# Kernel tuning notes

Hardware: AMD Instinct MI355X
Metric: run time of the kernel (lower is better)

## Reference

```python
import jax, jax.numpy as jnp
import numpy as np

B, N, C = 1, 131072, 128
BS, H = 32, 4          # block_size, num_heads
HD = C // H            # head_dim = 32
NB = N // BS           # num_blocks = 4096
NEG = -1e30            # stand-in for -inf (identical softmax result, safe grads)


def setup_inputs() -> dict:
    key = jax.random.key(0)
    ks = jax.random.split(key, 8)
    x = jax.random.normal(ks[0], (B, N, C), jnp.float32)
    edge_feats = jax.random.normal(ks[1], (NB, BS, BS + 1, 4), jnp.float32)
    # 0/1 connectivity mask; guarantee self (diagonal) and global-token column are attendable
    attn_mask = jax.random.randint(ks[2], (NB, BS, BS + 1), 0, 2).astype(jnp.int32)
    attn_mask = attn_mask.at[:, :, BS].set(1)
    d = jnp.arange(BS)
    attn_mask = attn_mask.at[:, d, d].set(1)
    # parameters (torch nn.Linear layout: weight [out, in])
    Wqkv = jax.random.normal(ks[3], (3 * C, C), jnp.float32) * (C ** -0.5)
    bqkv = jnp.zeros((3 * C,), jnp.float32)
    Wproj = jax.random.normal(ks[4], (C, C), jnp.float32) * (C ** -0.5)
    bproj = jnp.zeros((C,), jnp.float32)
    Wgate = jax.random.normal(ks[5], (H, 4), jnp.float32) * 0.01  # init std=0.01
    bgate = jnp.zeros((H,), jnp.float32)
    return dict(x=x, edge_feats=edge_feats, Wqkv=Wqkv, bqkv=bqkv,
                Wproj=Wproj, bproj=bproj, Wgate=Wgate, bgate=bgate,
                attn_mask=attn_mask)


def reference(x, edge_feats, Wqkv, bqkv, Wproj, bproj, Wgate, bgate, attn_mask):
    scale = HD ** -0.5
    x_blk = x.reshape(B, NB, BS, C)
    # global token per block = block mean
    block_node = x_blk.mean(axis=2, keepdims=True)          # [B,NB,1,C]
    kv = jnp.concatenate([x_blk, block_node], axis=2)       # [B,NB,BS+1,C]
    # qkv projections (slice the fused weight like the torch code slices outputs)
    q = (x_blk @ Wqkv[:C].T + bqkv[:C]).reshape(B, NB, BS, H, HD)
    k = (kv @ Wqkv[C:2 * C].T + bqkv[C:2 * C]).reshape(B, NB, BS + 1, H, HD)
    v = (kv @ Wqkv[2 * C:].T + bqkv[2 * C:]).reshape(B, NB, BS + 1, H, HD)
    scores = jnp.einsum('bnqhd,bnkhd->bnqkh', q, k) * scale  # [B,NB,BS,BS+1,H]
    # physics bias: overwrite global-token column and diagonal with (0,0,0,1)
    self_row = jnp.array([0.0, 0.0, 0.0, 1.0], jnp.float32)
    bp = jnp.broadcast_to(edge_feats[None], (B, NB, BS, BS + 1, 4))
    bp = bp.at[:, :, :, BS, :].set(self_row)
    d = jnp.arange(BS)
    bp = bp.at[:, :, d, d, :].set(self_row)
    scores = scores + bp[..., 3:4]                           # additive physics bias
    m = attn_mask[None, :, :, :, None] != 0                  # [1,NB,BS,BS+1,1]
    scores = jnp.where(m, scores, NEG)
    attn_probs = jax.nn.softmax(scores, axis=3)
    # additive edge gate (masked to 0 where disconnected)
    lew = jnp.where(m, bp @ Wgate.T + bgate, 0.0)            # [B,NB,BS,BS+1,H]
    combined = attn_probs + lew
    x_out = jnp.einsum('bnqkh,bnkhd->bnqhd', combined, v).reshape(B, N, C)
    return x_out @ Wproj.T + bproj
```

## Files before the change

### kernel.cpp

```cpp
#include <hip/hip_runtime.h>
#include <hip/hip_bf16.h>

#define NBLK 4096
#define BS 32
#define CH 128

typedef float f32x4 __attribute__((ext_vector_type(4)));
typedef int   i32x4 __attribute__((ext_vector_type(4)));
typedef short bf16x8 __attribute__((ext_vector_type(8)));
typedef unsigned short u16x4 __attribute__((ext_vector_type(4)));

__device__ __forceinline__ short f2b(float x) {
    return __builtin_bit_cast(short, __float2bfloat16(x));
}
__device__ __forceinline__ float b2f(unsigned short h) {
    union { unsigned u; float f; } c; c.u = ((unsigned)h) << 16; return c.f;
}
__device__ __forceinline__ u16x4 pack4(f32x4 a) {
    u16x4 o;
    o[0] = (unsigned short)f2b(a[0]); o[1] = (unsigned short)f2b(a[1]);
    o[2] = (unsigned short)f2b(a[2]); o[3] = (unsigned short)f2b(a[3]);
    return o;
}
__device__ __forceinline__ bf16x8 pack8(f32x4 a, f32x4 b) {
    bf16x8 o;
    o[0] = f2b(a[0]); o[1] = f2b(a[1]); o[2] = f2b(a[2]); o[3] = f2b(a[3]);
    o[4] = f2b(b[0]); o[5] = f2b(b[1]); o[6] = f2b(b[2]); o[7] = f2b(b[3]);
    return o;
}
__device__ __forceinline__ int swz(int row, int col) {
    return (row << 5) + ((((col >> 3) ^ ((row >> 1) & 3)) << 3) | (col & 7));
}

__global__ void convert_weights(const float* __restrict__ wqkv,
                                const float* __restrict__ wproj,
                                short* __restrict__ wsout) {
    int i = blockIdx.x * 256 + threadIdx.x;
    if (i < 3 * CH * CH) {
        wsout[i] = f2b(wqkv[i]);
    } else {
        int j = i - 3 * CH * CH;
        if (j < CH * CH) wsout[3 * CH * CH + j] = f2b(wproj[j]);
    }
}

__launch_bounds__(256, 3)
__global__ void fused_block_attn(
    const float* __restrict__ x,
    const float* __restrict__ edge_feats,
    const float* __restrict__ bqkv,
    const float* __restrict__ bproj,
    const float* __restrict__ wgate,
    const float* __restrict__ bgate,
    const int*   __restrict__ attn_mask,
    const short* __restrict__ wqkv_b,
    const short* __restrict__ wproj_b,
    float* __restrict__ out)
{
    const int b    = blockIdx.x;
    const int tid  = threadIdx.x;
    const int lane = tid & 63;
    const int w    = tid >> 6;
    const int lm   = lane & 15;
    const int g    = lane >> 4;
    const int ak   = g * 8;
    const int rb   = g * 4;

    __shared__ short Rv[4096];
    __shared__ short Rq[4096];
    __shared__ short Rk[4096];
    __shared__ short efS[4096];
    short* vt = Rv + w * 1024;
    short* qc = Rq + w * 1024;
    short* kc = Rk + w * 1024;

    const int pr = tid >> 3;
    const int pu = tid & 7;
    const float* efp = edge_feats + ((size_t)(b * BS + pr) * 33 + pu * 4) * 4;
    f32x4 efv[4];
    efv[0] = ((const f32x4*)efp)[0];
    efv[1] = ((const f32x4*)efp)[1];
    efv[2] = ((const f32x4*)efp)[2];
    efv[3] = ((const f32x4*)efp)[3];
    const i32x4 mkv = *(const i32x4*)(attn_mask + (size_t)(b * BS + pr) * 33 + pu * 4);

    const float* xb = x + (size_t)b * (BS * CH);
    bf16x8 kvf[2][4];
    #pragma unroll
    for (int kk = 0; kk < 4; ++kk) {
        const float* p0 = xb + lm * CH + kk * 32 + ak;
        const float* p1 = p0 + 16 * CH;
        kvf[0][kk] = pack8(*(const f32x4*)p0, *(const f32x4*)(p0 + 4));
        kvf[1][kk] = pack8(*(const f32x4*)p1, *(const f32x4*)(p1 + 4));
    }

    bf16x8 wfa[4][4];
    #pragma unroll
    for (int t = 0; t < 4; ++t) {
        const int o0 = ((t >> 1) ? CH : 0) + w * 32 + (t & 1) * 16;
        const short* wp = wqkv_b + (o0 + lm) * CH + ak;
        #pragma unroll
        for (int kk = 0; kk < 4; ++kk) wfa[t][kk] = *(const bf16x8*)(wp + kk * 32);
    }
    #pragma unroll
    for (int t = 0; t < 4; ++t) {
        const int o0 = ((t >> 1) ? CH : 0) + w * 32 + (t & 1) * 16;
        f32x4 acc0 = *(const f32x4*)(bqkv + o0 + rb);
        f32x4 acc1 = acc0;
        #pragma unroll
        for (int kk = 0; kk < 4; ++kk) {
            acc0 = __builtin_amdgcn_mfma_f32_16x16x32_bf16(wfa[t][kk], kvf[0][kk], acc0, 0, 0, 0);
            acc1 = __builtin_amdgcn_mfma_f32_16x16x32_bf16(wfa[t][kk], kvf[1][kk], acc1, 0, 0, 0);
        }
        short* dst = (t >> 1) ? kc : qc;
        const int c0 = (t & 1) * 16 + rb;
        *(u16x4*)&dst[swz(lm, c0)]      = pack4(acc0);
        *(u16x4*)&dst[swz(16 + lm, c0)] = pack4(acc1);
    }
    #pragma unroll
    for (int t = 0; t < 2; ++t) {
        const int o0 = 2 * CH + w * 32 + t * 16;
        const short* wp = wqkv_b + (o0 + lm) * CH + ak;
        bf16x8 wf[4];
        #pragma unroll
        for (int kk = 0; kk < 4; ++kk) wf[kk] = *(const bf16x8*)(wp + kk * 32);
        float bv = bqkv[o0 + lm];
        f32x4 acc0 = {bv, bv, bv, bv};
        f32x4 acc1 = acc0;
        #pragma unroll
        for (int kk = 0; kk < 4; ++kk) {
            acc0 = __builtin_amdgcn_mfma_f32_16x16x32_bf16(kvf[0][kk], wf[kk], acc0, 0, 0, 0);
            acc1 = __builtin_amdgcn_mfma_f32_16x16x32_bf16(kvf[1][kk], wf[kk], acc1, 0, 0, 0);
        }
        const int row = t * 16 + lm;
        *(u16x4*)&vt[swz(row, rb)]      = pack4(acc0);
        *(u16x4*)&vt[swz(row, 16 + rb)] = pack4(acc1);
    }

    {
        #pragma unroll
        for (int jj = 0; jj < 2; ++jj) {
            bf16x8 st;
            #pragma unroll
            for (int h2 = 0; h2 < 2; ++h2) {
                const int s = pu * 4 + jj * 2 + h2;
                f32x4 e = efv[jj * 2 + h2];
                if (s == pr) { e[0] = 0.f; e[1] = 0.f; e[2] = 0.f; e[3] = 1.f; }
                const float e3 = mkv[jj * 2 + h2] ? e[3] : -INFINITY;
                st[h2 * 4 + 0] = f2b(e[0]);
                st[h2 * 4 + 1] = f2b(e[1]);
                st[h2 * 4 + 2] = f2b(e[2]);
                st[h2 * 4 + 3] = f2b(e3);
            }
            const int chunk = pu * 2 + jj;
            *(bf16x8*)&efS[pr * 128 + ((chunk ^ (pr & 15)) << 3)] = st;
        }
    }
    __syncthreads();

    {
        bf16x8 af0 = *(const bf16x8*)&kc[swz(lm, ak)];
        bf16x8 af1 = *(const bf16x8*)&kc[swz(16 + lm, ak)];
        bf16x8 bq0 = *(const bf16x8*)&qc[swz(lm, ak)];
        bf16x8 bq1 = *(const bf16x8*)&qc[swz(16 + lm, ak)];
        f32x4 z = {0.f, 0.f, 0.f, 0.f};
        f32x4 s00 = __builtin_amdgcn_mfma_f32_16x16x32_bf16(af0, bq0, z, 0, 0, 0);
        f32x4 s10 = __builtin_amdgcn_mfma_f32_16x16x32_bf16(af1, bq0, z, 0, 0, 0);
        f32x4 s01 = __builtin_amdgcn_mfma_f32_16x16x32_bf16(af0, bq1, z, 0, 0, 0);
        f32x4 s11 = __builtin_amdgcn_mfma_f32_16x16x32_bf16(af1, bq1, z, 0, 0, 0);
        const float SC = 0.17677669529663689f;
        *(u16x4*)&kc[swz(lm, rb)]           = pack4(s00 * SC);
        *(u16x4*)&kc[swz(lm, 16 + rb)]      = pack4(s10 * SC);
        *(u16x4*)&kc[swz(16 + lm, rb)]      = pack4(s01 * SC);
        *(u16x4*)&kc[swz(16 + lm, 16 + rb)] = pack4(s11 * SC);
    }

    {
        const int r    = lane >> 1;
        const int half = lane & 1;
        bf16x8 t0 = *(const bf16x8*)&kc[swz(r, half * 16)];
        bf16x8 t1 = *(const bf16x8*)&kc[swz(r, half * 16 + 8)];

        float dv[16];
        #pragma unroll
        for (int j = 0; j < 8; ++j) {
            dv[j]     = b2f((unsigned short)t0[j]);
            dv[8 + j] = b2f((unsigned short)t1[j]);
        }
        float sd = 0.f;
        #pragma unroll
        for (int j = 0; j < 16; ++j) sd += dv[j];
        sd += __shfl_xor(sd, 1);
        const float d32 = sd * 0.03125f;

        f32x4 wg = *(const f32x4*)(wgate + w * 4);
        float bg = bgate[w];

        float e[16], lw[16];
        float se = 0.f;
        #pragma unroll
        for (int pk = 0; pk < 8; ++pk) {
            const int chunk = half * 8 + pk;
            bf16x8 c = *(const bf16x8*)&efS[r * 128 + ((chunk ^ (r & 15)) << 3)];
            #pragma unroll
            for (int h2 = 0; h2 < 2; ++h2) {
                const int idx = pk * 2 + h2;
                const float f0 = b2f((unsigned short)c[h2 * 4 + 0]);
                const float f1 = b2f((unsigned short)c[h2 * 4 + 1]);
                const float f2c = b2f((unsigned short)c[h2 * 4 + 2]);
                const float f3 = b2f((unsigned short)c[h2 * 4 + 3]);
                const bool m = f3 > -1.0e30f;
                lw[idx] = m ? (f0 * wg[0] + f1 * wg[1] + f2c * wg[2] + f3 * wg[3] + bg) : 0.f;
                e[idx]  = __expf(dv[idx] + f3);
                se += e[idx];
            }
        }
        const float e32 = __expf(d32 + 1.0f);
        const float tot = se + __shfl_xor(se, 1) + e32;
        const float rinv = 1.0f / tot;
        const float add32 = (e32 * rinv + wg[3] + bg) * 0.03125f;

        #pragma unroll
        for (int pk = 0; pk < 4; ++pk) {
            f32x4 v;
            #pragma unroll
            for (int j = 0; j < 4; ++j) {
                int idx = pk * 4 + j;
                v[j] = e[idx] * rinv + lw[idx] + add32;
            }
            *(u16x4*)&kc[swz(r, half * 16 + pk * 4)] = pack4(v);
        }
    }

    {
        bf16x8 av0 = *(const bf16x8*)&vt[swz(lm, ak)];
        bf16x8 av1 = *(const bf16x8*)&vt[swz(16 + lm, ak)];
        bf16x8 bc0 = *(const bf16x8*)&kc[swz(lm, ak)];
        bf16x8 bc1 = *(const bf16x8*)&kc[swz(16 + lm, ak)];
        f32x4 z = {0.f, 0.f, 0.f, 0.f};
        f32x4 x00 = __builtin_amdgcn_mfma_f32_16x16x32_bf16(av0, bc0, z, 0, 0, 0);
        f32x4 x10 = __builtin_amdgcn_mfma_f32_16x16x32_bf16(av1, bc0, z, 0, 0, 0);
        f32x4 x01 = __builtin_amdgcn_mfma_f32_16x16x32_bf16(av0, bc1, z, 0, 0, 0);
        f32x4 x11 = __builtin_amdgcn_mfma_f32_16x16x32_bf16(av1, bc1, z, 0, 0, 0);
        *(u16x4*)&qc[swz(lm, rb)]           = pack4(x00);
        *(u16x4*)&qc[swz(lm, 16 + rb)]      = pack4(x10);
        *(u16x4*)&qc[swz(16 + lm, rb)]      = pack4(x01);
        *(u16x4*)&qc[swz(16 + lm, 16 + rb)] = pack4(x11);
    }

    bf16x8 pw[2][4];
    float pb[2];
    #pragma unroll
    for (int t = 0; t < 2; ++t) {
        int col = w * 32 + t * 16 + lm;
        pb[t] = bproj[col];
        #pragma unroll
        for (int kk = 0; kk < 4; ++kk)
            pw[t][kk] = *(const bf16x8*)(wproj_b + col * CH + kk * 32 + ak);
    }
    __syncthreads();

    {
        bf16x8 a2[2][4];
        #pragma unroll
        for (int kk = 0; kk < 4; ++kk) {
            a2[0][kk] = *(const bf16x8*)&Rq[kk * 1024 + swz(lm, ak)];
            a2[1][kk] = *(const bf16x8*)&Rq[kk * 1024 + swz(16 + lm, ak)];
        }
        float* ob = out + (size_t)b * BS * CH;
        #pragma unroll
        for (int t = 0; t < 2; ++t) {
            int col = w * 32 + t * 16 + lm;
            f32x4 acc0 = {pb[t], pb[t], pb[t], pb[t]};
            f32x4 acc1 = acc0;
            #pragma unroll
            for (int kk = 0; kk < 4; ++kk) {
                acc0 = __builtin_amdgcn_mfma_f32_16x16x32_bf16(a2[0][kk], pw[t][kk], acc0, 0, 0, 0);
                acc1 = __builtin_amdgcn_mfma_f32_16x16x32_bf16(a2[1][kk], pw[t][kk], acc1, 0, 0, 0);
            }
            #pragma unroll
            for (int j = 0; j < 4; ++j) {
                ob[(rb + j) * CH + col]      = acc0[j];
                ob[(16 + rb + j) * CH + col] = acc1[j];
            }
        }
    }
}

extern "C" void kernel_launch(void* const* d_in, const int* in_sizes, int n_in,
                              void* d_out, int out_size, void* d_ws, size_t ws_size,
                              hipStream_t stream) {
    const float* x          = (const float*)d_in[0];
    const float* edge_feats = (const float*)d_in[1];
    const float* Wqkv       = (const float*)d_in[2];
    const float* bqkv       = (const float*)d_in[3];
    const float* Wproj      = (const float*)d_in[4];
    const float* bproj      = (const float*)d_in[5];
    const float* Wgate      = (const float*)d_in[6];
    const float* bgate      = (const float*)d_in[7];
    const int*   attn_mask  = (const int*)d_in[8];
    float* out = (float*)d_out;
    short* wb  = (short*)d_ws;

    convert_weights<<<256, 256, 0, stream>>>(Wqkv, Wproj, wb);
    fused_block_attn<<<NBLK, 256, 0, stream>>>(
        x, edge_feats, bqkv, bproj, Wgate, bgate, attn_mask,
        wb, wb + 3 * CH * CH, out);
}
```

Baseline: 107.8 us.

## Process two attention blocks per workgroup and keep V in registers via shuffles

Each workgroup now handles two consecutive 32-token blocks, so Wqkv and Wproj fragments loaded from global memory are reused across both blocks. The V tile is no longer staged in shared memory; it is kept packed in registers and redistributed into MFMA operand layout with cross-lane shuffles. This halves the grid size and doubles the shared memory per workgroup (Rq/Rk/efS now 16KB each), which may reduce occupancy under the 256x3 launch bound and raise register pressure.

```diff
diff --git a/kernel.cpp b/kernel.cpp
--- a/kernel.cpp
+++ b/kernel.cpp
@@ -7,6 +7,7 @@
 
 typedef float f32x4 __attribute__((ext_vector_type(4)));
 typedef int   i32x4 __attribute__((ext_vector_type(4)));
+typedef int   i32x2 __attribute__((ext_vector_type(2)));
 typedef short bf16x8 __attribute__((ext_vector_type(8)));
 typedef unsigned short u16x4 __attribute__((ext_vector_type(4)));
 
@@ -31,6 +32,7 @@
 __device__ __forceinline__ int swz(int row, int col) {
     return (row << 5) + ((((col >> 3) ^ ((row >> 1) & 3)) << 3) | (col & 7));
 }
+__device__ __forceinline__ int shfl64(int v, int sl) { return __shfl(v, sl, 64); }
 
 __global__ void convert_weights(const float* __restrict__ wqkv,
                                 const float* __restrict__ wproj,
@@ -57,7 +59,7 @@
     const short* __restrict__ wproj_b,
     float* __restrict__ out)
 {
-    const int b    = blockIdx.x;
+    const int bp   = blockIdx.x;
     const int tid  = threadIdx.x;
     const int lane = tid & 63;
     const int w    = tid >> 6;
@@ -66,57 +68,83 @@
     const int ak   = g * 8;
     const int rb   = g * 4;
 
-    __shared__ short Rv[4096];
-    __shared__ short Rq[4096];
-    __shared__ short Rk[4096];
-    __shared__ short efS[4096];
-    short* vt = Rv + w * 1024;
-    short* qc = Rq + w * 1024;
-    short* kc = Rk + w * 1024;
+    __shared__ short Rq[8192];
+    __shared__ short Rk[8192];
+    __shared__ short efS[8192];
 
     const int pr = tid >> 3;
     const int pu = tid & 7;
-    const float* efp = edge_feats + ((size_t)(b * BS + pr) * 33 + pu * 4) * 4;
-    f32x4 efv[4];
-    efv[0] = ((const f32x4*)efp)[0];
-    efv[1] = ((const f32x4*)efp)[1];
-    efv[2] = ((const f32x4*)efp)[2];
-    efv[3] = ((const f32x4*)efp)[3];
-    const i32x4 mkv = *(const i32x4*)(attn_mask + (size_t)(b * BS + pr) * 33 + pu * 4);
-
-    const float* xb = x + (size_t)b * (BS * CH);
-    bf16x8 kvf[2][4];
-    #pragma unroll
-    for (int kk = 0; kk < 4; ++kk) {
-        const float* p0 = xb + lm * CH + kk * 32 + ak;
-        const float* p1 = p0 + 16 * CH;
-        kvf[0][kk] = pack8(*(const f32x4*)p0, *(const f32x4*)(p0 + 4));
-        kvf[1][kk] = pack8(*(const f32x4*)p1, *(const f32x4*)(p1 + 4));
-    }
-
-    bf16x8 wfa[4][4];
+    {
+        f32x4 efv[2][4];
+        i32x4 mkv[2];
+        #pragma unroll
+        for (int blk = 0; blk < 2; ++blk) {
+            const size_t row = (size_t)((2 * bp + blk) * BS + pr);
+            const float* efp = edge_feats + (row * 33 + pu * 4) * 4;
+            efv[blk][0] = ((const f32x4*)efp)[0];
+            efv[blk][1] = ((const f32x4*)efp)[1];
+            efv[blk][2] = ((const f32x4*)efp)[2];
+            efv[blk][3] = ((const f32x4*)efp)[3];
+            mkv[blk] = *(const i32x4*)(attn_mask + row * 33 + pu * 4);
+        }
+        #pragma unroll
+        for (int blk = 0; blk < 2; ++blk) {
+            #pragma unroll
+            for (int jj = 0; jj < 2; ++jj) {
+                bf16x8 st;
+                #pragma unroll
+                for (int h2 = 0; h2 < 2; ++h2) {
+                    const int s = pu * 4 + jj * 2 + h2;
+                    f32x4 e = efv[blk][jj * 2 + h2];
+                    if (s == pr) { e[0] = 0.f; e[1] = 0.f; e[2] = 0.f; e[3] = 1.f; }
+                    const float e3 = mkv[blk][jj * 2 + h2] ? e[3] : -INFINITY;
+                    st[h2 * 4 + 0] = f2b(e[0]);
+                    st[h2 * 4 + 1] = f2b(e[1]);
+                    st[h2 * 4 + 2] = f2b(e[2]);
+                    st[h2 * 4 + 3] = f2b(e3);
+                }
+                const int chunk = pu * 2 + jj;
+                *(bf16x8*)&efS[blk * 4096 + pr * 128 + ((chunk ^ (pr & 15)) << 3)] = st;
+            }
+        }
+    }
+
+    bf16x8 kvf[2][2][4];
+    #pragma unroll
+    for (int blk = 0; blk < 2; ++blk) {
+        const float* xb = x + (size_t)(2 * bp + blk) * (BS * CH);
+        #pragma unroll
+        for (int kk = 0; kk < 4; ++kk) {
+            const float* p0 = xb + lm * CH + kk * 32 + ak;
+            const float* p1 = p0 + 16 * CH;
+            kvf[blk][0][kk] = pack8(*(const f32x4*)p0, *(const f32x4*)(p0 + 4));
+            kvf[blk][1][kk] = pack8(*(const f32x4*)p1, *(const f32x4*)(p1 + 4));
+        }
+    }
+
     #pragma unroll
     for (int t = 0; t < 4; ++t) {
         const int o0 = ((t >> 1) ? CH : 0) + w * 32 + (t & 1) * 16;
         const short* wp = wqkv_b + (o0 + lm) * CH + ak;
-        #pragma unroll
-        for (int kk = 0; kk < 4; ++kk) wfa[t][kk] = *(const bf16x8*)(wp + kk * 32);
-    }
-    #pragma unroll
-    for (int t = 0; t < 4; ++t) {
-        const int o0 = ((t >> 1) ? CH : 0) + w * 32 + (t & 1) * 16;
-        f32x4 acc0 = *(const f32x4*)(bqkv + o0 + rb);
-        f32x4 acc1 = acc0;
-        #pragma unroll
-        for (int kk = 0; kk < 4; ++kk) {
-            acc0 = __builtin_amdgcn_mfma_f32_16x16x32_bf16(wfa[t][kk], kvf[0][kk], acc0, 0, 0, 0);
-            acc1 = __builtin_amdgcn_mfma_f32_16x16x32_bf16(wfa[t][kk], kvf[1][kk], acc1, 0, 0, 0);
-        }
-        short* dst = (t >> 1) ? kc : qc;
-        const int c0 = (t & 1) * 16 + rb;
-        *(u16x4*)&dst[swz(lm, c0)]      = pack4(acc0);
-        *(u16x4*)&dst[swz(16 + lm, c0)] = pack4(acc1);
-    }
+        bf16x8 wf[4];
+        #pragma unroll
+        for (int kk = 0; kk < 4; ++kk) wf[kk] = *(const bf16x8*)(wp + kk * 32);
+        const f32x4 bias = *(const f32x4*)(bqkv + o0 + rb);
+        #pragma unroll
+        for (int blk = 0; blk < 2; ++blk) {
+            f32x4 acc0 = bias, acc1 = bias;
+            #pragma unroll
+            for (int kk = 0; kk < 4; ++kk) {
+                acc0 = __builtin_amdgcn_mfma_f32_16x16x32_bf16(wf[kk], kvf[blk][0][kk], acc0, 0, 0, 0);
+                acc1 = __builtin_amdgcn_mfma_f32_16x16x32_bf16(wf[kk], kvf[blk][1][kk], acc1, 0, 0, 0);
+            }
+            short* dst = ((t >> 1) ? Rk : Rq) + blk * 4096 + w * 1024;
+            const int c0 = (t & 1) * 16 + rb;
+            *(u16x4*)&dst[swz(lm, c0)]      = pack4(acc0);
+            *(u16x4*)&dst[swz(16 + lm, c0)] = pack4(acc1);
+        }
+    }
+    i32x2 vtp[2][2][2];
     #pragma unroll
     for (int t = 0; t < 2; ++t) {
         const int o0 = 2 * CH + w * 32 + t * 16;
@@ -124,41 +152,26 @@
         bf16x8 wf[4];
         #pragma unroll
         for (int kk = 0; kk < 4; ++kk) wf[kk] = *(const bf16x8*)(wp + kk * 32);
-        float bv = bqkv[o0 + lm];
-        f32x4 acc0 = {bv, bv, bv, bv};
-        f32x4 acc1 = acc0;
-        #pragma unroll
-        for (int kk = 0; kk < 4; ++kk) {
-            acc0 = __builtin_amdgcn_mfma_f32_16x16x32_bf16(kvf[0][kk], wf[kk], acc0, 0, 0, 0);
-            acc1 = __builtin_amdgcn_mfma_f32_16x16x32_bf16(kvf[1][kk], wf[kk], acc1, 0, 0, 0);
-        }
-        const int row = t * 16 + lm;
-        *(u16x4*)&vt[swz(row, rb)]      = pack4(acc0);
-        *(u16x4*)&vt[swz(row, 16 + rb)] = pack4(acc1);
-    }
-
-    {
-        #pragma unroll
-        for (int jj = 0; jj < 2; ++jj) {
-            bf16x8 st;
-            #pragma unroll
-            for (int h2 = 0; h2 < 2; ++h2) {
-                const int s = pu * 4 + jj * 2 + h2;
-                f32x4 e = efv[jj * 2 + h2];
-                if (s == pr) { e[0] = 0.f; e[1] = 0.f; e[2] = 0.f; e[3] = 1.f; }
-                const float e3 = mkv[jj * 2 + h2] ? e[3] : -INFINITY;
-                st[h2 * 4 + 0] = f2b(e[0]);
-                st[h2 * 4 + 1] = f2b(e[1]);
-                st[h2 * 4 + 2] = f2b(e[2]);
-                st[h2 * 4 + 3] = f2b(e3);
-            }
-            const int chunk = pu * 2 + jj;
-            *(bf16x8*)&efS[pr * 128 + ((chunk ^ (pr & 15)) << 3)] = st;
+        const float bv = bqkv[o0 + lm];
+        #pragma unroll
+        for (int blk = 0; blk < 2; ++blk) {
+            f32x4 acc0 = {bv, bv, bv, bv};
+            f32x4 acc1 = acc0;
+            #pragma unroll
+            for (int kk = 0; kk < 4; ++kk) {
+                acc0 = __builtin_amdgcn_mfma_f32_16x16x32_bf16(kvf[blk][0][kk], wf[kk], acc0, 0, 0, 0);
+                acc1 = __builtin_amdgcn_mfma_f32_16x16x32_bf16(kvf[blk][1][kk], wf[kk], acc1, 0, 0, 0);
+            }
+            vtp[blk][t][0] = __builtin_bit_cast(i32x2, pack4(acc0));
+            vtp[blk][t][1] = __builtin_bit_cast(i32x2, pack4(acc1));
         }
     }
     __syncthreads();
 
-    {
+    #pragma unroll
+    for (int blk = 0; blk < 2; ++blk) {
+        short* kc = Rk + blk * 4096 + w * 1024;
+        short* qc = Rq + blk * 4096 + w * 1024;
         bf16x8 af0 = *(const bf16x8*)&kc[swz(lm, ak)];
         bf16x8 af1 = *(const bf16x8*)&kc[swz(16 + lm, ak)];
         bf16x8 bq0 = *(const bf16x8*)&qc[swz(lm, ak)];
@@ -175,7 +188,10 @@
         *(u16x4*)&kc[swz(16 + lm, 16 + rb)] = pack4(s11 * SC);
     }
 
-    {
+    #pragma unroll
+    for (int blk = 0; blk < 2; ++blk) {
+        short* kc = Rk + blk * 4096 + w * 1024;
+        const short* efSb = efS + blk * 4096;
         const int r    = lane >> 1;
         const int half = lane & 1;
         bf16x8 t0 = *(const bf16x8*)&kc[swz(r, half * 16)];
@@ -201,7 +217,7 @@
         #pragma unroll
         for (int pk = 0; pk < 8; ++pk) {
             const int chunk = half * 8 + pk;
-            bf16x8 c = *(const bf16x8*)&efS[r * 128 + ((chunk ^ (r & 15)) << 3)];
+            bf16x8 c = *(const bf16x8*)&efSb[r * 128 + ((chunk ^ (r & 15)) << 3)];
             #pragma unroll
             for (int h2 = 0; h2 < 2; ++h2) {
                 const int idx = pk * 2 + h2;
@@ -232,16 +248,36 @@
         }
     }
 
-    {
-        bf16x8 av0 = *(const bf16x8*)&vt[swz(lm, ak)];
-        bf16x8 av1 = *(const bf16x8*)&vt[swz(16 + lm, ak)];
+    const int srcA = lm + 16 * ((2 * g) & 3);
+    const int srcB = lm + 16 * ((2 * g + 1) & 3);
+    #pragma unroll
+    for (int blk = 0; blk < 2; ++blk) {
+        short* kc = Rk + blk * 4096 + w * 1024;
+        short* qc = Rq + blk * 4096 + w * 1024;
+        bf16x8 av[2];
+        #pragma unroll
+        for (int t = 0; t < 2; ++t) {
+            const i32x2 pa = vtp[blk][t][0];
+            const i32x2 pb2 = vtp[blk][t][1];
+            const int a0x = shfl64(pa[0], srcA),  a0y = shfl64(pa[1], srcA);
+            const int a1x = shfl64(pb2[0], srcA), a1y = shfl64(pb2[1], srcA);
+            const int b0x = shfl64(pa[0], srcB),  b0y = shfl64(pa[1], srcB);
+            const int b1x = shfl64(pb2[0], srcB), b1y = shfl64(pb2[1], srcB);
+            const bool lo = (g < 2);
+            i32x4 wv;
+            wv[0] = lo ? a0x : a1x;
+            wv[1] = lo ? a0y : a1y;
+            wv[2] = lo ? b0x : b1x;
+            wv[3] = lo ? b0y : b1y;
+            av[t] = __builtin_bit_cast(bf16x8, wv);
+        }
         bf16x8 bc0 = *(const bf16x8*)&kc[swz(lm, ak)];
         bf16x8 bc1 = *(const bf16x8*)&kc[swz(16 + lm, ak)];
         f32x4 z = {0.f, 0.f, 0.f, 0.f};
-        f32x4 x00 = __builtin_amdgcn_mfma_f32_16x16x32_bf16(av0, bc0, z, 0, 0, 0);
-        f32x4 x10 = __builtin_amdgcn_mfma_f32_16x16x32_bf16(av1, bc0, z, 0, 0, 0);
-        f32x4 x01 = __builtin_amdgcn_mfma_f32_16x16x32_bf16(av0, bc1, z, 0, 0, 0);
-        f32x4 x11 = __builtin_amdgcn_mfma_f32_16x16x32_bf16(av1, bc1, z, 0, 0, 0);
+        f32x4 x00 = __builtin_amdgcn_mfma_f32_16x16x32_bf16(av[0], bc0, z, 0, 0, 0);
+        f32x4 x10 = __builtin_amdgcn_mfma_f32_16x16x32_bf16(av[1], bc0, z, 0, 0, 0);
+        f32x4 x01 = __builtin_amdgcn_mfma_f32_16x16x32_bf16(av[0], bc1, z, 0, 0, 0);
+        f32x4 x11 = __builtin_amdgcn_mfma_f32_16x16x32_bf16(av[1], bc1, z, 0, 0, 0);
         *(u16x4*)&qc[swz(lm, rb)]           = pack4(x00);
         *(u16x4*)&qc[swz(lm, 16 + rb)]      = pack4(x10);
         *(u16x4*)&qc[swz(16 + lm, rb)]      = pack4(x01);
@@ -260,14 +296,15 @@
     }
     __syncthreads();
 
-    {
+    #pragma unroll
+    for (int blk = 0; blk < 2; ++blk) {
         bf16x8 a2[2][4];
         #pragma unroll
         for (int kk = 0; kk < 4; ++kk) {
-            a2[0][kk] = *(const bf16x8*)&Rq[kk * 1024 + swz(lm, ak)];
-            a2[1][kk] = *(const bf16x8*)&Rq[kk * 1024 + swz(16 + lm, ak)];
-        }
-        float* ob = out + (size_t)b * BS * CH;
+            a2[0][kk] = *(const bf16x8*)&Rq[blk * 4096 + kk * 1024 + swz(lm, ak)];
+            a2[1][kk] = *(const bf16x8*)&Rq[blk * 4096 + kk * 1024 + swz(16 + lm, ak)];
+        }
+        float* ob = out + (size_t)(2 * bp + blk) * BS * CH;
         #pragma unroll
         for (int t = 0; t < 2; ++t) {
             int col = w * 32 + t * 16 + lm;
@@ -303,7 +340,7 @@
     short* wb  = (short*)d_ws;
 
     convert_weights<<<256, 256, 0, stream>>>(Wqkv, Wproj, wb);
-    fused_block_attn<<<NBLK, 256, 0, stream>>>(
+    fused_block_attn<<<NBLK / 2, 256, 0, stream>>>(
         x, edge_feats, bqkv, bproj, Wgate, bgate, attn_mask,
         wb, wb + 3 * CH * CH, out);
 }
```

After: 91.61 us. 1.18x faster.
